# Performance work log

Measured on AMD Instinct MI355X. Metric: run time of the kernel, lower is better.

The kernel has to match this reference:

```python
import math
import jax, jax.numpy as jnp
import numpy as np

B, T, C, H = 2, 2048, 1024, 16

def setup_inputs() -> dict:
    key = jax.random.key(0)
    k1, k2, k3 = jax.random.split(key, 3)
    x = jax.random.normal(k1, (B, T, C), dtype=jnp.float32)
    W_kqv = jax.random.normal(k2, (C, 3 * C), dtype=jnp.float32) * (1.0 / math.sqrt(C))
    W_proj = jax.random.normal(k3, (C, C), dtype=jnp.float32) * (1.0 / math.sqrt(C))
    b_proj = jnp.zeros((C,), dtype=jnp.float32)
    return {"x": x, "W_kqv": W_kqv, "W_proj": W_proj, "b_proj": b_proj}

def reference(x, W_kqv, W_proj, b_proj):
    Bx, Tx, Cx = x.shape
    hs = Cx // H  # head size
    q, k, v = jnp.split(x @ W_kqv, 3, axis=2)  # each (B,T,C)
    # (B,T,C) -> (B,H,T,hs)
    q = q.reshape(Bx, Tx, H, hs).transpose(0, 2, 1, 3)
    k = k.reshape(Bx, Tx, H, hs).transpose(0, 2, 1, 3)
    v = v.reshape(Bx, Tx, H, hs).transpose(0, 2, 1, 3)
    attn = jnp.einsum('bhqd,bhkd->bhqk', q, k) / math.sqrt(hs)  # (B,H,T,T)
    causal = jnp.tril(jnp.ones((Tx, Tx), dtype=bool))
    attn = jnp.where(causal, attn, -jnp.inf)
    attn = jax.nn.softmax(attn, axis=-1)
    y = jnp.einsum('bhqk,bhkd->bhqd', attn, v)  # (B,H,T,hs)
    y = y.transpose(0, 2, 1, 3).reshape(Bx, Tx, Cx)
    return y @ W_proj + b_proj
```

## Files before the change

kernel.cpp:

```cpp
#include <hip/hip_runtime.h>


typedef unsigned short u16;
typedef unsigned int u32;
typedef __bf16 bf16x8 __attribute__((ext_vector_type(8)));
typedef float f32x4 __attribute__((ext_vector_type(4)));
typedef u32 u32x4 __attribute__((ext_vector_type(4)));
typedef u32 u32x2 __attribute__((ext_vector_type(2)));
typedef u16 u16x4 __attribute__((ext_vector_type(4)));

__device__ __forceinline__ u16 f2bf(float f) {
  u32 u = __float_as_uint(f);
  u32 r = u + 0x7FFFu + ((u >> 16) & 1u);
  return (u16)(r >> 16);
}

__device__ __forceinline__ u32 cvt_pk_bf16(float a, float b) {
  u32 r;
  asm("v_cvt_pk_bf16_f32 %0, %1, %2" : "=v"(r) : "v"(a), "v"(b));
  return r;
}

__device__ __forceinline__ bf16x8 ld_bf8(const u16* p) {
  union { u32x4 u; bf16x8 b; } x;
  x.u = *(const u32x4*)p;
  return x.b;
}

__device__ __forceinline__ void gld_lds16(const u16* g, u16* l) {
  __builtin_amdgcn_global_load_lds(
      (const __attribute__((address_space(1))) u32*)g,
      (__attribute__((address_space(3))) u32*)l, 16, 0, 0);
}

__device__ __forceinline__ void convT_body(const float* __restrict__ src,
                                           u16* __restrict__ dst, int R, int Cc,
                                           int r0, int c0, float* ls ) {
  int t = threadIdx.x;
  for (int u = t; u < 1024; u += 256) {
    int r = u >> 4, cs = (u & 15) << 2;
    float4 v = *(const float4*)&src[(size_t)(r0 + r) * Cc + (c0 + cs)];
    ls[r * 65 + cs] = v.x; ls[r * 65 + cs + 1] = v.y;
    ls[r * 65 + cs + 2] = v.z; ls[r * 65 + cs + 3] = v.w;
  }
  __syncthreads();
  for (int u = t; u < 1024; u += 256) {
    int n = u >> 4, ks = (u & 15) << 2;
    u16x4 o;
    o.x = f2bf(ls[ks * 65 + n]); o.y = f2bf(ls[(ks + 1) * 65 + n]);
    o.z = f2bf(ls[(ks + 2) * 65 + n]); o.w = f2bf(ls[(ks + 3) * 65 + n]);
    *(u16x4*)&dst[(size_t)(c0 + n) * R + (r0 + ks)] = o;
  }
}

__global__ __launch_bounds__(256) void prep_kernel(
    const float* __restrict__ x, const float* __restrict__ Wkqv,
    const float* __restrict__ Wproj, u16* __restrict__ xb,
    u16* __restrict__ wkqvT, u16* __restrict__ wprojT) {
  __shared__ float ls[64 * 65];
  int bx = blockIdx.x;
  if (bx < 2048) {
    int idx = bx * 256 + threadIdx.x;
    const float4* s4 = (const float4*)x;
    float4 a = s4[2 * idx], b = s4[2 * idx + 1];
    union { u16 h[8]; u32x4 v; } pk;
    pk.h[0] = f2bf(a.x); pk.h[1] = f2bf(a.y); pk.h[2] = f2bf(a.z); pk.h[3] = f2bf(a.w);
    pk.h[4] = f2bf(b.x); pk.h[5] = f2bf(b.y); pk.h[6] = f2bf(b.z); pk.h[7] = f2bf(b.w);
    *(u32x4*)&xb[(size_t)idx * 8] = pk.v;
  } else if (bx < 2816) {
    int idx = bx - 2048;
    convT_body(Wkqv, wkqvT, 1024, 3072, (idx & 15) * 64, (idx >> 4) * 64, ls);
  } else {
    int idx = bx - 2816;
    convT_body(Wproj, wprojT, 1024, 1024, (idx & 15) * 64, (idx >> 4) * 64, ls);
  }
}

__global__ __launch_bounds__(256) void qkv_gemm_kernel(
    const u16* __restrict__ A, const u16* __restrict__ Bt,
    u16* __restrict__ Qh, u16* __restrict__ Kh, u16* __restrict__ Vh, float qscale) {
  constexpr int K = 1024;
  __shared__ __align__(16) u16 As[128 * 32];
  __shared__ __align__(16) u16 Bs[128 * 32];
  int t = threadIdx.x;
  int wave = t >> 6, lane = t & 63, quad = lane >> 4, l16 = lane & 15;
  int wm = (wave >> 1) << 6, wn = (wave & 1) << 6;
  int m0 = blockIdx.x * 128, n0 = blockIdx.y * 128;
  f32x4 acc[4][4] = {};
  int u0 = t, u1 = t + 256;
  int ra0 = u0 >> 2, ca0 = ((u0 & 3) ^ ((u0 >> 3) & 3)) << 3;
  int ra1 = u1 >> 2, ca1 = ((u1 & 3) ^ ((u1 >> 3) & 3)) << 3;
  int swq = (quad ^ ((l16 >> 1) & 3)) << 3;
  for (int k0 = 0; k0 < K; k0 += 32) {
    gld_lds16(&A[(size_t)(m0 + ra0) * K + k0 + ca0], &As[u0 * 8]);
    gld_lds16(&A[(size_t)(m0 + ra1) * K + k0 + ca1], &As[u1 * 8]);
    gld_lds16(&Bt[(size_t)(n0 + ra0) * K + k0 + ca0], &Bs[u0 * 8]);
    gld_lds16(&Bt[(size_t)(n0 + ra1) * K + k0 + ca1], &Bs[u1 * 8]);
    __syncthreads();
    bf16x8 af[4], bfr[4];
    for (int r = 0; r < 4; ++r) af[r] = ld_bf8(&As[(wm + r * 16 + l16) * 32 + swq]);
    for (int c = 0; c < 4; ++c) bfr[c] = ld_bf8(&Bs[(wn + c * 16 + l16) * 32 + swq]);
    for (int r = 0; r < 4; ++r)
      for (int c = 0; c < 4; ++c)
        acc[r][c] = __builtin_amdgcn_mfma_f32_16x16x32_bf16(af[r], bfr[c], acc[r][c], 0, 0, 0);
    __syncthreads();
  }
  for (int r = 0; r < 4; ++r) {
    int rowbase = m0 + wm + r * 16 + quad * 4;
    for (int c = 0; c < 4; ++c) {
      int col = n0 + wn + c * 16 + l16;
      int seg = col >> 10;
      int cc = col & 1023;
      int h = cc >> 6, d = cc & 63;
      for (int i = 0; i < 4; ++i) {
        int row = rowbase + i;
        int b = row >> 11, tt = row & 2047;
        size_t off = (((size_t)(b * 16 + h)) * 2048 + tt) * 64 + d;
        float v = acc[r][c][i];
        if (seg == 0)      Qh[off] = f2bf(v * qscale);
        else if (seg == 1) Kh[off] = f2bf(v);
        else               Vh[off] = f2bf(v);
      }
    }
  }
}

__global__ __launch_bounds__(256) void vT_kernel(const u16* __restrict__ Vh,
                                                 u16* __restrict__ Vt) {
  __shared__ __align__(16) u16 ls[64 * 72];
  int t = threadIdx.x;
  int t0 = blockIdx.x * 64, bh = blockIdx.y;
  const u16* in = Vh + ((size_t)bh * 2048 + t0) * 64;
  for (int u = t; u < 512; u += 256) {
    int row = u >> 3, col = (u & 7) << 3;
    *(u32x4*)&ls[row * 72 + col] = *(const u32x4*)&in[(size_t)row * 64 + col];
  }
  __syncthreads();
  for (int u = t; u < 512; u += 256) {
    int d = u >> 3, tc = (u & 7) << 3;
    union { u16 h[8]; u32x4 v; } pk;
    for (int j = 0; j < 8; ++j) pk.h[j] = ls[(tc + j) * 72 + d];
    *(u32x4*)&Vt[((size_t)bh * 64 + d) * 2048 + t0 + tc] = pk.v;
  }
}

__global__ __launch_bounds__(256) void proj_gemm_kernel(
    const u16* __restrict__ A, const u16* __restrict__ Bt,
    float* __restrict__ out, const float* __restrict__ bias) {
  constexpr int K = 1024;
  __shared__ __align__(16) u16 As[64 * 32];
  __shared__ __align__(16) u16 Bs[64 * 32];
  int t = threadIdx.x;
  int wave = t >> 6, lane = t & 63, quad = lane >> 4, l16 = lane & 15;
  int wm = (wave >> 1) << 5, wn = (wave & 1) << 5;
  int m0 = blockIdx.x * 64, n0 = blockIdx.y * 64;
  f32x4 acc[2][2] = {};
  int u0 = t;
  int ra0 = u0 >> 2, ca0 = ((u0 & 3) ^ ((u0 >> 3) & 3)) << 3;
  int swq = (quad ^ ((l16 >> 1) & 3)) << 3;
  for (int k0 = 0; k0 < K; k0 += 32) {
    gld_lds16(&A[(size_t)(m0 + ra0) * K + k0 + ca0], &As[u0 * 8]);
    gld_lds16(&Bt[(size_t)(n0 + ra0) * K + k0 + ca0], &Bs[u0 * 8]);
    __syncthreads();
    bf16x8 af[2], bfr[2];
    for (int r = 0; r < 2; ++r) af[r] = ld_bf8(&As[(wm + r * 16 + l16) * 32 + swq]);
    for (int c = 0; c < 2; ++c) bfr[c] = ld_bf8(&Bs[(wn + c * 16 + l16) * 32 + swq]);
    for (int r = 0; r < 2; ++r)
      for (int c = 0; c < 2; ++c)
        acc[r][c] = __builtin_amdgcn_mfma_f32_16x16x32_bf16(af[r], bfr[c], acc[r][c], 0, 0, 0);
    __syncthreads();
  }
  for (int r = 0; r < 2; ++r) {
    int rowbase = m0 + wm + r * 16 + quad * 4;
    for (int c = 0; c < 2; ++c) {
      int col = n0 + wn + c * 16 + l16;
      float bv = bias[col];
      for (int i = 0; i < 4; ++i)
        out[(size_t)(rowbase + i) * 1024 + col] = acc[r][c][i] + bv;
    }
  }
}

__global__ __launch_bounds__(256, 6) void flash_kernel(
    const u16* __restrict__ Qh, const u16* __restrict__ Kh, const u16* __restrict__ Vt,
    u16* __restrict__ yb, float* __restrict__ Opart) {
  __shared__ __align__(16) u16 Ks[64 * 64];
  __shared__ __align__(16) u16 Vs[64 * 64];
  int t = threadIdx.x, wave = t >> 6, lane = t & 63, quad = lane >> 4, l16 = lane & 15;
  int id = blockIdx.x;
  int g = id / 360, r = id % 360;
  int bh = g * 8 + (r & 7);
  int jx = r >> 3;
  int qtile, kvs, kve, sidx = 0, half = 0;
  bool partial;
  if (jx < 19) {
    qtile = 18 - jx; kvs = 0; kve = qtile + 1; partial = false;
  } else {
    sidx = (jx - 19) >> 1; half = (jx - 19) & 1;
    qtile = 31 - sidx;
    int nkv = qtile + 1, mid = nkv >> 1;
    kvs = half ? mid : 0; kve = half ? nkv : mid; partial = true;
  }
  int q0 = qtile << 6;
  const u16* Qb = Qh + (size_t)bh * 2048 * 64;
  const u16* Kb = Kh + (size_t)bh * 2048 * 64;
  const u16* Vb = Vt + (size_t)bh * 64 * 2048;
  bf16x8 qa0, qa1;
  {
    int qrow = q0 + wave * 16 + l16;
    qa0 = ld_bf8(&Qb[(size_t)qrow * 64 + quad * 8]);
    qa1 = ld_bf8(&Qb[(size_t)qrow * 64 + 32 + quad * 8]);
  }
  f32x4 oacc[4] = {};
  float lsum = 0.f;
  int u0 = wave * 128 + lane, u1 = u0 + 64;
  int r0 = u0 >> 3, p0 = u0 & 7, cb0 = (p0 - r0) & 7;
  int r1s = u1 >> 3, p1 = u1 & 7, cb1 = (p1 - r1s) & 7;
  int vsub = (quad & 1) * 4;
  int vc0 = quad >> 1;
  for (int j = kvs; j < kve; ++j) {
    int kv0 = j << 6;
    __syncthreads();
    gld_lds16(&Kb[(size_t)(kv0 + r0) * 64 + cb0 * 8], &Ks[u0 * 8]);
    gld_lds16(&Kb[(size_t)(kv0 + r1s) * 64 + cb1 * 8], &Ks[u1 * 8]);
    gld_lds16(&Vb[(size_t)r0 * 2048 + kv0 + cb0 * 8], &Vs[u0 * 8]);
    gld_lds16(&Vb[(size_t)r1s * 2048 + kv0 + cb1 * 8], &Vs[u1 * 8]);
    __syncthreads();
    bool maskit = (j == qtile);
    u32 w[4][2];
    for (int c = 0; c < 4; ++c) {
      int krow = c * 16 + l16;
      bf16x8 kb0 = ld_bf8(&Ks[krow * 64 + ((quad + krow) & 7) * 8]);
      bf16x8 kb1 = ld_bf8(&Ks[krow * 64 + ((quad + 4 + krow) & 7) * 8]);
      f32x4 z = {0.f, 0.f, 0.f, 0.f};
      z = __builtin_amdgcn_mfma_f32_16x16x32_bf16(kb0, qa0, z, 0, 0, 0);
      z = __builtin_amdgcn_mfma_f32_16x16x32_bf16(kb1, qa1, z, 0, 0, 0);
      float pexp[4];
      if (maskit) {
        int qg = q0 + wave * 16 + l16;
        for (int i = 0; i < 4; ++i) {
          float p = __builtin_amdgcn_exp2f(z[i]);
          if (kv0 + c * 16 + quad * 4 + i > qg) p = 0.f;
          lsum += p;
          pexp[i] = p;
        }
      } else {
        for (int i = 0; i < 4; ++i) {
          float p = __builtin_amdgcn_exp2f(z[i]);
          lsum += p;
          pexp[i] = p;
        }
      }
      w[c][0] = cvt_pk_bf16(pexp[0], pexp[1]);
      w[c][1] = cvt_pk_bf16(pexp[2], pexp[3]);
    }
    union { u32 uu[4]; bf16x8 b; } pf0, pf1;
    pf0.uu[0] = w[0][0]; pf0.uu[1] = w[0][1]; pf0.uu[2] = w[1][0]; pf0.uu[3] = w[1][1];
    pf1.uu[0] = w[2][0]; pf1.uu[1] = w[2][1]; pf1.uu[2] = w[3][0]; pf1.uu[3] = w[3][1];
    for (int dt = 0; dt < 4; ++dt) {
      int vrow = dt * 16 + l16;
      int rbase = vrow * 64 + vsub;
      union { u32x2 lo2; struct { u32 a, b; }; } h0lo, h0hi, h1lo, h1hi;
      h0lo.lo2 = *(const u32x2*)&Vs[rbase + (((vc0)     + vrow) & 7) * 8];
      h0hi.lo2 = *(const u32x2*)&Vs[rbase + (((vc0 + 2) + vrow) & 7) * 8];
      h1lo.lo2 = *(const u32x2*)&Vs[rbase + (((vc0 + 4) + vrow) & 7) * 8];
      h1hi.lo2 = *(const u32x2*)&Vs[rbase + (((vc0 + 6) + vrow) & 7) * 8];
      union { u32 uu[4]; bf16x8 b; } va0, va1;
      va0.uu[0] = h0lo.a; va0.uu[1] = h0lo.b; va0.uu[2] = h0hi.a; va0.uu[3] = h0hi.b;
      va1.uu[0] = h1lo.a; va1.uu[1] = h1lo.b; va1.uu[2] = h1hi.a; va1.uu[3] = h1hi.b;
      oacc[dt] = __builtin_amdgcn_mfma_f32_16x16x32_bf16(va0.b, pf0.b, oacc[dt], 0, 0, 0);
      oacc[dt] = __builtin_amdgcn_mfma_f32_16x16x32_bf16(va1.b, pf1.b, oacc[dt], 0, 0, 0);
    }
  }
  lsum += __shfl_xor(lsum, 16);
  lsum += __shfl_xor(lsum, 32);
  if (partial) {
    float* Op = Opart + ((size_t)(bh * 13 + sidx) * 2 + half) * 4160;
    int qloc = wave * 16 + l16;
    for (int dt = 0; dt < 4; ++dt)
      *(f32x4*)&Op[qloc * 64 + dt * 16 + quad * 4] = oacc[dt];
    if (quad == 0) Op[4096 + qloc] = lsum;
  } else {
    int b = bh >> 4, hd = bh & 15;
    float inv = 1.0f / lsum;
    int qq = q0 + wave * 16 + l16;
    size_t rowoff = ((size_t)(b * 2048 + qq)) * 1024 + hd * 64;
    for (int dt = 0; dt < 4; ++dt) {
      u32x2 pr;
      pr.x = cvt_pk_bf16(oacc[dt][0] * inv, oacc[dt][1] * inv);
      pr.y = cvt_pk_bf16(oacc[dt][2] * inv, oacc[dt][3] * inv);
      *(u32x2*)&yb[rowoff + dt * 16 + quad * 4] = pr;
    }
  }
}

__global__ __launch_bounds__(256) void combine_kernel(const float* __restrict__ Opart,
                                                      u16* __restrict__ yb) {
  int sidx = blockIdx.x, bh = blockIdx.y, t = threadIdx.x;
  int qtile = 31 - sidx;
  const float* A = Opart + (size_t)(bh * 13 + sidx) * 2 * 4160;
  const float* Bp = A + 4160;
  int q = t >> 2, d0 = (t & 3) << 4;
  float inv = 1.0f / (A[4096 + q] + Bp[4096 + q]);
  int b = bh >> 4, h = bh & 15;
  size_t off = ((size_t)(b * 2048 + (qtile << 6) + q)) * 1024 + h * 64 + d0;
  union { u16 hh[16]; u32x4 v[2]; } pk;
  for (int k = 0; k < 16; ++k)
    pk.hh[k] = f2bf((A[q * 64 + d0 + k] + Bp[q * 64 + d0 + k]) * inv);
  *(u32x4*)&yb[off] = pk.v[0];
  *(u32x4*)&yb[off + 8] = pk.v[1];
}

extern "C" void kernel_launch(void* const* d_in, const int* in_sizes, int n_in,
                              void* d_out, int out_size, void* d_ws, size_t ws_size,
                              hipStream_t stream) {
  const float* x     = (const float*)d_in[0];
  const float* Wkqv  = (const float*)d_in[1];
  const float* Wproj = (const float*)d_in[2];
  const float* bproj = (const float*)d_in[3];
  float* out = (float*)d_out;

  u16* ws     = (u16*)d_ws;
  u16* xb     = ws;
  u16* wkqvT  = xb + (size_t)4096 * 1024;
  u16* wprojT = wkqvT + (size_t)3072 * 1024;
  u16* Qh     = wprojT + (size_t)1024 * 1024;
  u16* Kh     = Qh + (size_t)32 * 2048 * 64;
  u16* Vt     = Kh + (size_t)32 * 2048 * 64;
  u16* yb     = Vt + (size_t)32 * 2048 * 64;
  u16* Vh     = yb;
  float* Opart = (float*)ws;

  const float QSCALE = 0.18033688011112042f;

  prep_kernel<<<3072, 256, 0, stream>>>(x, Wkqv, Wproj, xb, wkqvT, wprojT);
  qkv_gemm_kernel<<<dim3(32, 24), 256, 0, stream>>>(xb, wkqvT, Qh, Kh, Vh, QSCALE);
  vT_kernel<<<dim3(32, 32), 256, 0, stream>>>(Vh, Vt);
  flash_kernel<<<1440, 256, 0, stream>>>(Qh, Kh, Vt, yb, Opart);
  combine_kernel<<<dim3(13, 32), 256, 0, stream>>>(Opart, yb);
  proj_gemm_kernel<<<dim3(64, 16), 256, 0, stream>>>(yb, wprojT, out, bproj);
}
```

Before: 181.0 us.

## Double flash-attention query tile to 128 rows per block for K/V reuse

Each wave now handles 32 query rows (two 16-row MFMA tiles) instead of 16, so each K/V tile loaded into LDS feeds twice as many MFMAs. The work schedule is re-encoded with a lookup table over 16 query tiles, splitting the largest 6 tiles into two KV halves, and the combine kernel is resized to match. Waves whose rows lie entirely above the current KV tile now skip compute. This cuts K/V load and sync overhead per FLOP, at the cost of more registers (launch bound lowered to 4 blocks) and fewer, coarser blocks, which may hurt load balance.

```diff
diff --git a/kernel.cpp b/kernel.cpp
--- a/kernel.cpp
+++ b/kernel.cpp
@@ -181,38 +181,43 @@
   }
 }
 
-__global__ __launch_bounds__(256, 6) void flash_kernel(
+__global__ __launch_bounds__(256, 4) void flash_kernel(
     const u16* __restrict__ Qh, const u16* __restrict__ Kh, const u16* __restrict__ Vt,
     u16* __restrict__ yb, float* __restrict__ Opart) {
   __shared__ __align__(16) u16 Ks[64 * 64];
   __shared__ __align__(16) u16 Vs[64 * 64];
   int t = threadIdx.x, wave = t >> 6, lane = t & 63, quad = lane >> 4, l16 = lane & 15;
+  const unsigned char JT[22] = {9, 8, 7, 47, 63, 46, 62, 6, 45, 61, 44, 60,
+                                5, 43, 59, 42, 58, 4, 3, 2, 1, 0};
   int id = blockIdx.x;
-  int g = id / 360, r = id % 360;
+  int g = id / 176, r = id % 176;
   int bh = g * 8 + (r & 7);
   int jx = r >> 3;
-  int qtile, kvs, kve, sidx = 0, half = 0;
-  bool partial;
-  if (jx < 19) {
-    qtile = 18 - jx; kvs = 0; kve = qtile + 1; partial = false;
-  } else {
-    sidx = (jx - 19) >> 1; half = (jx - 19) & 1;
-    qtile = 31 - sidx;
-    int nkv = qtile + 1, mid = nkv >> 1;
-    kvs = half ? mid : 0; kve = half ? nkv : mid; partial = true;
-  }
-  int q0 = qtile << 6;
+  int code = JT[jx];
+  int qtile = code & 15;
+  int half = (code >> 4) & 1;
+  bool partial = (code >> 5) != 0;
+  int nkv = 2 * qtile + 2, mid = qtile + 1;
+  int kvs = (partial && half) ? mid : 0;
+  int kve = partial ? (half ? nkv : mid) : nkv;
+  int sidx = 15 - qtile;
+  int q0 = qtile << 7;
   const u16* Qb = Qh + (size_t)bh * 2048 * 64;
   const u16* Kb = Kh + (size_t)bh * 2048 * 64;
   const u16* Vb = Vt + (size_t)bh * 64 * 2048;
-  bf16x8 qa0, qa1;
+  int qlo = q0 + wave * 32;
+  int qhi = qlo + 31;
+  bf16x8 qa0, qa1, qa2, qa3;
   {
-    int qrow = q0 + wave * 16 + l16;
-    qa0 = ld_bf8(&Qb[(size_t)qrow * 64 + quad * 8]);
-    qa1 = ld_bf8(&Qb[(size_t)qrow * 64 + 32 + quad * 8]);
-  }
-  f32x4 oacc[4] = {};
-  float lsum = 0.f;
+    int qr0 = qlo + l16;
+    qa0 = ld_bf8(&Qb[(size_t)qr0 * 64 + quad * 8]);
+    qa1 = ld_bf8(&Qb[(size_t)qr0 * 64 + 32 + quad * 8]);
+    int qr1 = qr0 + 16;
+    qa2 = ld_bf8(&Qb[(size_t)qr1 * 64 + quad * 8]);
+    qa3 = ld_bf8(&Qb[(size_t)qr1 * 64 + 32 + quad * 8]);
+  }
+  f32x4 oacc0[4] = {}, oacc1[4] = {};
+  float lsum0 = 0.f, lsum1 = 0.f;
   int u0 = wave * 128 + lane, u1 = u0 + 64;
   int r0 = u0 >> 3, p0 = u0 & 7, cb0 = (p0 - r0) & 7;
   int r1s = u1 >> 3, p1 = u1 & 7, cb1 = (p1 - r1s) & 7;
@@ -226,37 +231,46 @@
     gld_lds16(&Vb[(size_t)r0 * 2048 + kv0 + cb0 * 8], &Vs[u0 * 8]);
     gld_lds16(&Vb[(size_t)r1s * 2048 + kv0 + cb1 * 8], &Vs[u1 * 8]);
     __syncthreads();
-    bool maskit = (j == qtile);
-    u32 w[4][2];
+    if (kv0 > qhi) continue;
+    bool maskit = (kv0 + 63 > qlo);
+    u32 w0[4][2], w1[4][2];
     for (int c = 0; c < 4; ++c) {
       int krow = c * 16 + l16;
       bf16x8 kb0 = ld_bf8(&Ks[krow * 64 + ((quad + krow) & 7) * 8]);
       bf16x8 kb1 = ld_bf8(&Ks[krow * 64 + ((quad + 4 + krow) & 7) * 8]);
-      f32x4 z = {0.f, 0.f, 0.f, 0.f};
-      z = __builtin_amdgcn_mfma_f32_16x16x32_bf16(kb0, qa0, z, 0, 0, 0);
-      z = __builtin_amdgcn_mfma_f32_16x16x32_bf16(kb1, qa1, z, 0, 0, 0);
-      float pexp[4];
+      f32x4 z0 = {0.f, 0.f, 0.f, 0.f}, z1 = {0.f, 0.f, 0.f, 0.f};
+      z0 = __builtin_amdgcn_mfma_f32_16x16x32_bf16(kb0, qa0, z0, 0, 0, 0);
+      z0 = __builtin_amdgcn_mfma_f32_16x16x32_bf16(kb1, qa1, z0, 0, 0, 0);
+      z1 = __builtin_amdgcn_mfma_f32_16x16x32_bf16(kb0, qa2, z1, 0, 0, 0);
+      z1 = __builtin_amdgcn_mfma_f32_16x16x32_bf16(kb1, qa3, z1, 0, 0, 0);
+      float pe0[4], pe1[4];
       if (maskit) {
-        int qg = q0 + wave * 16 + l16;
+        int qg0 = qlo + l16, qg1 = qg0 + 16;
         for (int i = 0; i < 4; ++i) {
-          float p = __builtin_amdgcn_exp2f(z[i]);
-          if (kv0 + c * 16 + quad * 4 + i > qg) p = 0.f;
-          lsum += p;
-          pexp[i] = p;
+          int kv = kv0 + c * 16 + quad * 4 + i;
+          float a = __builtin_amdgcn_exp2f(z0[i]);
+          float b = __builtin_amdgcn_exp2f(z1[i]);
+          if (kv > qg0) a = 0.f;
+          if (kv > qg1) b = 0.f;
+          lsum0 += a; lsum1 += b;
+          pe0[i] = a; pe1[i] = b;
         }
       } else {
         for (int i = 0; i < 4; ++i) {
-          float p = __builtin_amdgcn_exp2f(z[i]);
-          lsum += p;
-          pexp[i] = p;
+          float a = __builtin_amdgcn_exp2f(z0[i]);
+          float b = __builtin_amdgcn_exp2f(z1[i]);
+          lsum0 += a; lsum1 += b;
+          pe0[i] = a; pe1[i] = b;
         }
       }
-      w[c][0] = cvt_pk_bf16(pexp[0], pexp[1]);
-      w[c][1] = cvt_pk_bf16(pexp[2], pexp[3]);
-    }
-    union { u32 uu[4]; bf16x8 b; } pf0, pf1;
-    pf0.uu[0] = w[0][0]; pf0.uu[1] = w[0][1]; pf0.uu[2] = w[1][0]; pf0.uu[3] = w[1][1];
-    pf1.uu[0] = w[2][0]; pf1.uu[1] = w[2][1]; pf1.uu[2] = w[3][0]; pf1.uu[3] = w[3][1];
+      w0[c][0] = cvt_pk_bf16(pe0[0], pe0[1]); w0[c][1] = cvt_pk_bf16(pe0[2], pe0[3]);
+      w1[c][0] = cvt_pk_bf16(pe1[0], pe1[1]); w1[c][1] = cvt_pk_bf16(pe1[2], pe1[3]);
+    }
+    union { u32 uu[4]; bf16x8 b; } pf00, pf01, pf10, pf11;
+    pf00.uu[0] = w0[0][0]; pf00.uu[1] = w0[0][1]; pf00.uu[2] = w0[1][0]; pf00.uu[3] = w0[1][1];
+    pf01.uu[0] = w0[2][0]; pf01.uu[1] = w0[2][1]; pf01.uu[2] = w0[3][0]; pf01.uu[3] = w0[3][1];
+    pf10.uu[0] = w1[0][0]; pf10.uu[1] = w1[0][1]; pf10.uu[2] = w1[1][0]; pf10.uu[3] = w1[1][1];
+    pf11.uu[0] = w1[2][0]; pf11.uu[1] = w1[2][1]; pf11.uu[2] = w1[3][0]; pf11.uu[3] = w1[3][1];
     for (int dt = 0; dt < 4; ++dt) {
       int vrow = dt * 16 + l16;
       int rbase = vrow * 64 + vsub;
@@ -268,28 +282,38 @@
       union { u32 uu[4]; bf16x8 b; } va0, va1;
       va0.uu[0] = h0lo.a; va0.uu[1] = h0lo.b; va0.uu[2] = h0hi.a; va0.uu[3] = h0hi.b;
       va1.uu[0] = h1lo.a; va1.uu[1] = h1lo.b; va1.uu[2] = h1hi.a; va1.uu[3] = h1hi.b;
-      oacc[dt] = __builtin_amdgcn_mfma_f32_16x16x32_bf16(va0.b, pf0.b, oacc[dt], 0, 0, 0);
-      oacc[dt] = __builtin_amdgcn_mfma_f32_16x16x32_bf16(va1.b, pf1.b, oacc[dt], 0, 0, 0);
-    }
-  }
-  lsum += __shfl_xor(lsum, 16);
-  lsum += __shfl_xor(lsum, 32);
+      oacc0[dt] = __builtin_amdgcn_mfma_f32_16x16x32_bf16(va0.b, pf00.b, oacc0[dt], 0, 0, 0);
+      oacc0[dt] = __builtin_amdgcn_mfma_f32_16x16x32_bf16(va1.b, pf01.b, oacc0[dt], 0, 0, 0);
+      oacc1[dt] = __builtin_amdgcn_mfma_f32_16x16x32_bf16(va0.b, pf10.b, oacc1[dt], 0, 0, 0);
+      oacc1[dt] = __builtin_amdgcn_mfma_f32_16x16x32_bf16(va1.b, pf11.b, oacc1[dt], 0, 0, 0);
+    }
+  }
+  lsum0 += __shfl_xor(lsum0, 16);
+  lsum0 += __shfl_xor(lsum0, 32);
+  lsum1 += __shfl_xor(lsum1, 16);
+  lsum1 += __shfl_xor(lsum1, 32);
   if (partial) {
-    float* Op = Opart + ((size_t)(bh * 13 + sidx) * 2 + half) * 4160;
-    int qloc = wave * 16 + l16;
+    float* Op = Opart + ((size_t)(bh * 6 + sidx) * 2 + half) * 8320;
+    int ql = wave * 32 + l16;
     for (int dt = 0; dt < 4; ++dt)
-      *(f32x4*)&Op[qloc * 64 + dt * 16 + quad * 4] = oacc[dt];
-    if (quad == 0) Op[4096 + qloc] = lsum;
+      *(f32x4*)&Op[ql * 64 + dt * 16 + quad * 4] = oacc0[dt];
+    for (int dt = 0; dt < 4; ++dt)
+      *(f32x4*)&Op[(ql + 16) * 64 + dt * 16 + quad * 4] = oacc1[dt];
+    if (quad == 0) { Op[8192 + ql] = lsum0; Op[8192 + ql + 16] = lsum1; }
   } else {
     int b = bh >> 4, hd = bh & 15;
-    float inv = 1.0f / lsum;
-    int qq = q0 + wave * 16 + l16;
-    size_t rowoff = ((size_t)(b * 2048 + qq)) * 1024 + hd * 64;
+    float inv0 = 1.0f / lsum0, inv1 = 1.0f / lsum1;
+    int qq0 = qlo + l16;
+    size_t ro0 = ((size_t)(b * 2048 + qq0)) * 1024 + hd * 64;
+    size_t ro1 = ro0 + (size_t)16 * 1024;
     for (int dt = 0; dt < 4; ++dt) {
       u32x2 pr;
-      pr.x = cvt_pk_bf16(oacc[dt][0] * inv, oacc[dt][1] * inv);
-      pr.y = cvt_pk_bf16(oacc[dt][2] * inv, oacc[dt][3] * inv);
-      *(u32x2*)&yb[rowoff + dt * 16 + quad * 4] = pr;
+      pr.x = cvt_pk_bf16(oacc0[dt][0] * inv0, oacc0[dt][1] * inv0);
+      pr.y = cvt_pk_bf16(oacc0[dt][2] * inv0, oacc0[dt][3] * inv0);
+      *(u32x2*)&yb[ro0 + dt * 16 + quad * 4] = pr;
+      pr.x = cvt_pk_bf16(oacc1[dt][0] * inv1, oacc1[dt][1] * inv1);
+      pr.y = cvt_pk_bf16(oacc1[dt][2] * inv1, oacc1[dt][3] * inv1);
+      *(u32x2*)&yb[ro1 + dt * 16 + quad * 4] = pr;
     }
   }
 }
@@ -297,18 +321,18 @@
 __global__ __launch_bounds__(256) void combine_kernel(const float* __restrict__ Opart,
                                                       u16* __restrict__ yb) {
   int sidx = blockIdx.x, bh = blockIdx.y, t = threadIdx.x;
-  int qtile = 31 - sidx;
-  const float* A = Opart + (size_t)(bh * 13 + sidx) * 2 * 4160;
-  const float* Bp = A + 4160;
-  int q = t >> 2, d0 = (t & 3) << 4;
-  float inv = 1.0f / (A[4096 + q] + Bp[4096 + q]);
+  int qtile = 15 - sidx;
+  const float* A = Opart + (size_t)(bh * 6 + sidx) * 2 * 8320;
+  const float* Bp = A + 8320;
+  int q = t >> 1, d0 = (t & 1) << 5;
+  float inv = 1.0f / (A[8192 + q] + Bp[8192 + q]);
   int b = bh >> 4, h = bh & 15;
-  size_t off = ((size_t)(b * 2048 + (qtile << 6) + q)) * 1024 + h * 64 + d0;
-  union { u16 hh[16]; u32x4 v[2]; } pk;
-  for (int k = 0; k < 16; ++k)
+  size_t off = ((size_t)(b * 2048 + (qtile << 7) + q)) * 1024 + h * 64 + d0;
+  union { u16 hh[32]; u32x4 v[4]; } pk;
+  for (int k = 0; k < 32; ++k)
     pk.hh[k] = f2bf((A[q * 64 + d0 + k] + Bp[q * 64 + d0 + k]) * inv);
-  *(u32x4*)&yb[off] = pk.v[0];
-  *(u32x4*)&yb[off + 8] = pk.v[1];
+  for (int s = 0; s < 4; ++s)
+    *(u32x4*)&yb[off + s * 8] = pk.v[s];
 }
 
 extern "C" void kernel_launch(void* const* d_in, const int* in_sizes, int n_in,
@@ -336,7 +360,7 @@
   prep_kernel<<<3072, 256, 0, stream>>>(x, Wkqv, Wproj, xb, wkqvT, wprojT);
   qkv_gemm_kernel<<<dim3(32, 24), 256, 0, stream>>>(xb, wkqvT, Qh, Kh, Vh, QSCALE);
   vT_kernel<<<dim3(32, 32), 256, 0, stream>>>(Vh, Vt);
-  flash_kernel<<<1440, 256, 0, stream>>>(Qh, Kh, Vt, yb, Opart);
-  combine_kernel<<<dim3(13, 32), 256, 0, stream>>>(Opart, yb);
+  flash_kernel<<<704, 256, 0, stream>>>(Qh, Kh, Vt, yb, Opart);
+  combine_kernel<<<dim3(6, 32), 256, 0, stream>>>(Opart, yb);
   proj_gemm_kernel<<<dim3(64, 16), 256, 0, stream>>>(yb, wprojT, out, bproj);
 }
```

Measured after the change: 181.4 us. No clear change (+0.2%).
